# Kernel tuning notes

Hardware: AMD Instinct MI355X
Metric: run time of the kernel (lower is better)

The kernel has to match this reference:

```python
import jax, jax.numpy as jnp
import numpy as np

D_IN, HID, HEADS, MAXN, OUT, B = 16, 128, 4, 8, 128, 32768
HD = HID // HEADS
EPS = 1e-5


def _ln(x, g, b):
    m = jnp.mean(x, -1, keepdims=True)
    v = jnp.mean((x - m) ** 2, -1, keepdims=True)
    return (x - m) * jax.lax.rsqrt(v + EPS) * g + b


def _encode(x, enc_w1, enc_b1, enc_g1, enc_be1, enc_w2, enc_b2, enc_g2, enc_be2):
    h = _ln(x @ enc_w1.T + enc_b1, enc_g1, enc_be1)
    h = jax.nn.relu(h)
    return _ln(h @ enc_w2.T + enc_b2, enc_g2, enc_be2)


def setup_inputs() -> dict:
    key = jax.random.key(0)
    ks = jax.random.split(key, 12)

    def xavier(k, shape):
        # xavier_uniform with gain=0.5, matching _init_weights
        lim = 0.5 * np.sqrt(6.0 / (shape[0] + shape[1]))
        return jax.random.uniform(k, shape, jnp.float32, -lim, lim)

    z = lambda n: jnp.zeros((n,), jnp.float32)
    o = lambda n: jnp.ones((n,), jnp.float32)
    return {
        "current_node": jax.random.normal(ks[0], (B, D_IN), jnp.float32),
        "neighbor_nodes": jax.random.normal(ks[1], (B, MAXN, D_IN), jnp.float32),
        "neighbor_mask": jax.random.randint(ks[2], (B, MAXN), 0, 2, jnp.int32),
        "enc_w1": xavier(ks[3], (HID, D_IN)), "enc_b1": z(HID),
        "enc_g1": o(HID), "enc_be1": z(HID),
        "enc_w2": xavier(ks[4], (HID, HID)), "enc_b2": z(HID),
        "enc_g2": o(HID), "enc_be2": z(HID),
        "in_proj_w": xavier(ks[5], (3 * HID, HID)), "in_proj_b": z(3 * HID),
        "out_w": xavier(ks[6], (HID, HID)), "out_b": z(HID),
        "an_g": o(HID), "an_b": z(HID),
        "p1_w": xavier(ks[7], (HID, 2 * HID)), "p1_b": z(HID),
        "p1_g": o(HID), "p1_be": z(HID),
        "p2_w": xavier(ks[8], (OUT, HID)), "p2_b": z(OUT),
        "p2_g": o(OUT), "p2_be": z(OUT),
    }


def _forward(current_node, neighbor_nodes, neighbor_mask,
             enc_w1, enc_b1, enc_g1, enc_be1, enc_w2, enc_b2, enc_g2, enc_be2,
             in_proj_w, in_proj_b, out_w, out_b, an_g, an_b,
             p1_w, p1_b, p1_g, p1_be, p2_w, p2_b, p2_g, p2_be):
    bsz = current_node.shape[0]
    cur_emb = _encode(current_node, enc_w1, enc_b1, enc_g1, enc_be1,
                      enc_w2, enc_b2, enc_g2, enc_be2)                  # [B, HID]
    nb_emb = _encode(neighbor_nodes, enc_w1, enc_b1, enc_g1, enc_be1,
                     enc_w2, enc_b2, enc_g2, enc_be2)                   # [B, N, HID]

    valid = neighbor_mask > 0                                            # [B, N]
    has_nb = jnp.any(valid, axis=1)                                      # [B]

    # MultiheadAttention (eval mode, dropout inactive): q from current node, k/v from neighbors
    wq, wk, wv = in_proj_w[:HID], in_proj_w[HID:2 * HID], in_proj_w[2 * HID:]
    bq, bk, bv = in_proj_b[:HID], in_proj_b[HID:2 * HID], in_proj_b[2 * HID:]
    q = (cur_emb @ wq.T + bq).reshape(bsz, HEADS, HD)                    # [B, H, hd]
    k = (nb_emb @ wk.T + bk).reshape(bsz, MAXN, HEADS, HD)               # [B, N, H, hd]
    v = (nb_emb @ wv.T + bv).reshape(bsz, MAXN, HEADS, HD)

    scores = jnp.einsum('bhd,bnhd->bhn', q, k) / np.sqrt(HD)             # [B, H, N]
    # rows with zero valid neighbors get a fully-open mask to avoid NaN softmax;
    # their attention result is discarded below (replaced by cur_emb)
    safe = jnp.where(has_nb[:, None], valid, True)                       # [B, N]
    scores = jnp.where(safe[:, None, :], scores, -1e9)
    attn = jax.nn.softmax(scores, axis=-1)                               # [B, H, N]
    ctx = jnp.einsum('bhn,bnhd->bhd', attn, v).reshape(bsz, HID)
    ctx = ctx @ out_w.T + out_b
    agg = jnp.where(has_nb[:, None], _ln(ctx, an_g, an_b), cur_emb)      # [B, HID]

    combined = jnp.concatenate([cur_emb, agg], axis=-1)                  # [B, 2*HID]
    h = _ln(combined @ p1_w.T + p1_b, p1_g, p1_be)
    h = jax.nn.relu(h)
    return _ln(h @ p2_w.T + p2_b, p2_g, p2_be)                           # [B, OUT]


def reference(current_node, neighbor_nodes, neighbor_mask,
              enc_w1, enc_b1, enc_g1, enc_be1, enc_w2, enc_b2, enc_g2, enc_be2,
              in_proj_w, in_proj_b, out_w, out_b, an_g, an_b,
              p1_w, p1_b, p1_g, p1_be, p2_w, p2_b, p2_g, p2_be):
    return _forward(current_node, neighbor_nodes, neighbor_mask,
                    enc_w1, enc_b1, enc_g1, enc_be1, enc_w2, enc_b2, enc_g2, enc_be2,
                    in_proj_w, in_proj_b, out_w, out_b, an_g, an_b,
                    p1_w, p1_b, p1_g, p1_be, p2_w, p2_b, p2_g, p2_be)
```

## Files before the change

kernel.cpp:

```cpp
#include <hip/hip_runtime.h>

#define DEV __device__ __forceinline__

typedef __attribute__((ext_vector_type(8))) short bf16x8;
typedef __attribute__((ext_vector_type(4))) float f32x4;

static constexpr int NTH = 512;
static constexpr int TBE = 16;

static constexpr int W1P = 0;
static constexpr int W2  = 4096;
static constexpr int WQ  = 20480;
static constexpr int WK  = 36864;
static constexpr int WVW = 53248;
static constexpr int OW  = 69632;
static constexpr int P1A = 86016;
static constexpr int P1B = 102400;
static constexpr int P2W = 118784;
static constexpr int WS_BF16_TOT = 135168;
static constexpr int NPRM = 18 * 128;
static constexpr int WQr  = 139776;
static constexpr int OWr  = 156160;
static constexpr int P1Ar = 172544;
static constexpr int P1Br = 188928;
static constexpr int P2r  = 205312;
static constexpr int WKt  = 221696;
static constexpr int CURE = 238080;
static constexpr int NBE  = 238080 + 4194304;
static constexpr size_t SPLIT_NEED = (size_t)(NBE + 33554432) * 2;

DEV unsigned short f2bf(float f) {
  unsigned u = __float_as_uint(f);
  return (unsigned short)((u + 0x7fffu + ((u >> 16) & 1u)) >> 16);
}
DEV float bf2f(unsigned short u) { return __uint_as_float(((unsigned)u) << 16); }

DEV void st_bf16(unsigned short* buf, int row, int col, float v) {
  buf[row * 128 + ((((col >> 3) ^ (row & 7)) << 3) | (col & 7))] = f2bf(v);
}
DEV float ld_bf16(const unsigned short* buf, int row, int col) {
  unsigned u = buf[row * 128 + ((((col >> 3) ^ (row & 7)) << 3) | (col & 7))];
  return __uint_as_float(u << 16);
}
DEV bf16x8 frag128(const unsigned short* buf, int row, int kk, int lg) {
  return *(const bf16x8*)(buf + row * 128 + (((kk * 4 + lg) ^ (row & 7)) << 3));
}
DEV bf16x8 frag32(const unsigned short* buf, int row, int lg) {
  return *(const bf16x8*)(buf + row * 32 + ((lg ^ (row & 3)) << 3));
}
DEV f32x4 mfma16(bf16x8 a, bf16x8 b, f32x4 c) {
  return __builtin_amdgcn_mfma_f32_16x16x32_bf16(a, b, c, 0, 0, 0);
}

__global__ void prep(const float* __restrict__ enc_w1, const float* __restrict__ enc_w2,
                     const float* __restrict__ in_pw, const float* __restrict__ out_w,
                     const float* __restrict__ p1_w, const float* __restrict__ p2_w,
                     const float* __restrict__ enc_b1, const float* __restrict__ enc_g1,
                     const float* __restrict__ enc_be1, const float* __restrict__ enc_b2,
                     const float* __restrict__ enc_g2, const float* __restrict__ enc_be2,
                     const float* __restrict__ in_pb, const float* __restrict__ out_b,
                     const float* __restrict__ an_g, const float* __restrict__ an_b,
                     const float* __restrict__ p1_b, const float* __restrict__ p1_g,
                     const float* __restrict__ p1_be, const float* __restrict__ p2_b,
                     const float* __restrict__ p2_g, const float* __restrict__ p2_be,
                     unsigned short* __restrict__ wsb, float* __restrict__ wsp, int rm) {
  int t = blockIdx.x * blockDim.x + threadIdx.x;
  int NT = gridDim.x * blockDim.x;
  for (int i = t; i < 8 * 16384; i += NT) {
    int mi = i >> 14, e = i & 16383, row = e >> 7, col = e & 127;
    float v; int dstb;
    switch (mi) {
      case 0: v = enc_w2[row * 128 + col];         dstb = W2;  break;
      case 1: v = in_pw[row * 128 + col];          dstb = WQ;  break;
      case 2: v = in_pw[(128 + row) * 128 + col];  dstb = WK;  break;
      case 3: v = in_pw[(256 + row) * 128 + col];  dstb = WVW; break;
      case 4: v = out_w[row * 128 + col];          dstb = OW;  break;
      case 5: v = p1_w[row * 256 + col];           dstb = P1A; break;
      case 6: v = p1_w[row * 256 + 128 + col];     dstb = P1B; break;
      default: v = p2_w[row * 128 + col];          dstb = P2W; break;
    }
    wsb[dstb + row * 128 + ((((col >> 3) ^ (row & 7)) << 3) | (col & 7))] = f2bf(v);
  }
  for (int i = t; i < 4096; i += NT) {
    int row = i >> 5, col = i & 31;
    float v = (col < 16) ? enc_w1[row * 16 + col] : 0.f;
    wsb[W1P + row * 32 + ((((col >> 3) ^ (row & 3)) << 3) | (col & 7))] = f2bf(v);
  }
  if (rm) {
    for (int i = t; i < 6 * 16384; i += NT) {
      int mi = i >> 14, e = i & 16383, row = e >> 7, col = e & 127;
      float v; int dstb;
      switch (mi) {
        case 0: v = in_pw[row * 128 + col];         dstb = WQr;  break;
        case 1: v = out_w[row * 128 + col];         dstb = OWr;  break;
        case 2: v = p1_w[row * 256 + col];          dstb = P1Ar; break;
        case 3: v = p1_w[row * 256 + 128 + col];    dstb = P1Br; break;
        case 4: v = p2_w[row * 128 + col];          dstb = P2r;  break;
        default: v = in_pw[(128 + col) * 128 + row]; dstb = WKt; break;
      }
      wsb[dstb + e] = f2bf(v);
    }
  }
  for (int i = t; i < NPRM; i += NT) {
    int s = i >> 7, c = i & 127; float v;
    switch (s) {
      case 0: v = enc_b1[c]; break;  case 1: v = enc_g1[c]; break;
      case 2: v = enc_be1[c]; break; case 3: v = enc_b2[c]; break;
      case 4: v = enc_g2[c]; break;  case 5: v = enc_be2[c]; break;
      case 6: v = in_pb[c]; break;   case 7: v = in_pb[128 + c]; break;
      case 8: v = in_pb[256 + c]; break; case 9: v = out_b[c]; break;
      case 10: v = an_g[c]; break;   case 11: v = an_b[c]; break;
      case 12: v = p1_b[c]; break;   case 13: v = p1_g[c]; break;
      case 14: v = p1_be[c]; break;  case 15: v = p2_b[c]; break;
      case 16: v = p2_g[c]; break;   default: v = p2_be[c]; break;
    }
    wsp[i] = v;
  }
}

__global__ __launch_bounds__(512, 4)
void k1_enc(const float* __restrict__ cur_x, const float* __restrict__ nb_x,
            const unsigned short* __restrict__ wsb, const float* __restrict__ wsp,
            unsigned short* __restrict__ wse) {
  __shared__ __align__(16) unsigned short s_w1[4096];
  __shared__ __align__(16) unsigned short s_w2[16384];
  __shared__ __align__(16) unsigned short s_h1[8][16 * 136];
  __shared__ float s_prm[6 * 128];

  const int tid = threadIdx.x;
  const int wv = tid >> 6, l = tid & 63, l15 = l & 15, lg = l >> 4;

  ((uint4*)s_w1)[tid] = ((const uint4*)(wsb + W1P))[tid];
#pragma unroll
  for (int i = 0; i < 4; ++i)
    ((uint4*)s_w2)[tid + i * 512] = ((const uint4*)(wsb + W2))[tid + i * 512];
  for (int i = tid; i < 768; i += 512) s_prm[i] = wsp[i];
  __syncthreads();

  unsigned short* h1 = &s_h1[wv][0];

  auto ln_t = [&](float (&acc)[8][4], int bs, int gs, int es, bool relu) {
#pragma unroll
    for (int ct = 0; ct < 8; ++ct) {
      float4 bb = *(const float4*)&s_prm[bs * 128 + ct * 16 + lg * 4];
      acc[ct][0] += bb.x; acc[ct][1] += bb.y; acc[ct][2] += bb.z; acc[ct][3] += bb.w;
    }
    float sm = 0.f, sq = 0.f;
#pragma unroll
    for (int ct = 0; ct < 8; ++ct)
#pragma unroll
      for (int r = 0; r < 4; ++r) { sm += acc[ct][r]; sq = fmaf(acc[ct][r], acc[ct][r], sq); }
    sm += __shfl_xor(sm, 16); sq += __shfl_xor(sq, 16);
    sm += __shfl_xor(sm, 32); sq += __shfl_xor(sq, 32);
    float mean = sm * 0.0078125f;
    float var = fmaf(sq, 0.0078125f, -mean * mean);
    float inv = rsqrtf(var + 1e-5f);
#pragma unroll
    for (int ct = 0; ct < 8; ++ct) {
      float4 gg = *(const float4*)&s_prm[gs * 128 + ct * 16 + lg * 4];
      float4 ee = *(const float4*)&s_prm[es * 128 + ct * 16 + lg * 4];
      float ga[4] = {gg.x, gg.y, gg.z, gg.w}, ea[4] = {ee.x, ee.y, ee.z, ee.w};
#pragma unroll
      for (int r = 0; r < 4; ++r) {
        float v = (acc[ct][r] - mean) * inv * ga[r] + ea[r];
        acc[ct][r] = relu ? fmaxf(v, 0.f) : v;
      }
    }
  };

#pragma unroll 1
  for (int t = blockIdx.x * 8 + wv; t < 18432; t += 9216) {
    asm volatile("s_waitcnt lgkmcnt(0)" ::: "memory");
    const bool isnb = t < 16384;
    const float* src = isnb ? nb_x + (size_t)t * 256
                            : cur_x + ((size_t)t - 16384) * 256;
    unsigned short* dst = wse + (isnb ? (size_t)NBE + (size_t)t * 2048
                                      : (size_t)CURE + ((size_t)t - 16384) * 2048);

    float4 fin = ((const float4*)src)[l];
    {
      uint2 u;
      u.x = (unsigned)f2bf(fin.x) | ((unsigned)f2bf(fin.y) << 16);
      u.y = (unsigned)f2bf(fin.z) | ((unsigned)f2bf(fin.w) << 16);
      *(uint2*)(h1 + (l >> 2) * 16 + (l & 3) * 4) = u;
    }
    bf16x8 bx = (bf16x8){0, 0, 0, 0, 0, 0, 0, 0};
    if (lg < 2) bx = *(const bf16x8*)(h1 + l15 * 16 + lg * 8);

    float acc[8][4];
#pragma unroll
    for (int ct = 0; ct < 8; ++ct) {
      f32x4 a = {0.f, 0.f, 0.f, 0.f};
      a = mfma16(frag32(s_w1, ct * 16 + l15, lg), bx, a);
      acc[ct][0] = a[0]; acc[ct][1] = a[1]; acc[ct][2] = a[2]; acc[ct][3] = a[3];
    }
    ln_t(acc, 0, 1, 2, true);
#pragma unroll
    for (int ct = 0; ct < 8; ++ct) {
      uint2 u;
      u.x = (unsigned)f2bf(acc[ct][0]) | ((unsigned)f2bf(acc[ct][1]) << 16);
      u.y = (unsigned)f2bf(acc[ct][2]) | ((unsigned)f2bf(acc[ct][3]) << 16);
      *(uint2*)(h1 + l15 * 136 + ct * 16 + lg * 4) = u;
    }

    bf16x8 bh[4];
#pragma unroll
    for (int kk = 0; kk < 4; ++kk)
      bh[kk] = *(const bf16x8*)(h1 + l15 * 136 + kk * 32 + lg * 8);
#pragma unroll
    for (int ct = 0; ct < 8; ++ct) {
      f32x4 a = {0.f, 0.f, 0.f, 0.f};
#pragma unroll
      for (int kk = 0; kk < 4; ++kk)
        a = mfma16(frag128(s_w2, ct * 16 + l15, kk, lg), bh[kk], a);
      acc[ct][0] = a[0]; acc[ct][1] = a[1]; acc[ct][2] = a[2]; acc[ct][3] = a[3];
    }
    ln_t(acc, 3, 4, 5, false);

#pragma unroll
    for (int ct = 0; ct < 8; ++ct) {
      uint2 u;
      u.x = (unsigned)f2bf(acc[ct][0]) | ((unsigned)f2bf(acc[ct][1]) << 16);
      u.y = (unsigned)f2bf(acc[ct][2]) | ((unsigned)f2bf(acc[ct][3]) << 16);
      int c = ct * 2 + (lg >> 1);
      *(uint2*)(h1 + l15 * 128 + ((c ^ l15) << 3) + (lg & 1) * 4) = u;
    }
#pragma unroll
    for (int i = 0; i < 4; ++i) {
      int R = i * 4 + lg;
      int j = l15;
      uint4 u = *(const uint4*)(h1 + R * 128 + ((j ^ R) << 3));
      ((uint4*)dst)[i * 64 + l] = u;
    }
  }
}

__global__ __launch_bounds__(256, 2)
void k2_head(const int* __restrict__ nb_mask,
             const unsigned short* __restrict__ wsb, const float* __restrict__ wsp,
             float* __restrict__ out) {
  __shared__ __align__(16) unsigned char smem[47936];
  unsigned short* s_stage = (unsigned short*)smem;
  float*          s_f     = (float*)smem;
  unsigned short* s_agg   = (unsigned short*)(smem + 8448);
  unsigned short* s_q     = (unsigned short*)(smem + 32768);
  unsigned short* s_hh    = (unsigned short*)(smem + 32768);
  unsigned short* s_cur   = (unsigned short*)(smem + 37120);
  unsigned short* s_ctx   = (unsigned short*)(smem + 41472);
  float*          s_p     = (float*)(smem + 45824);
  int*            s_mask  = (int*)(smem + 47872);

  const int tid = threadIdx.x;
  const int wv = tid >> 6, l = tid & 63, l15 = l & 15, lg = l >> 4;
  const int ebase = blockIdx.x * TBE;

  {
    int row = tid >> 4, chunk = tid & 15;
    ((uint4*)s_cur)[row * 17 + chunk] = ((const uint4*)(wsb + CURE))[(size_t)ebase * 16 + tid];
  }
  if (tid < 16) {
    int m = 0; const int* mp = nb_mask + (size_t)(ebase + tid) * 8;
#pragma unroll
    for (int n = 0; n < 8; ++n) m |= (mp[n] > 0) << n;
    s_mask[tid] = m;
  }
  __syncthreads();

  {
    bf16x8 a[4];
#pragma unroll
    for (int kk = 0; kk < 4; ++kk)
      a[kk] = *(const bf16x8*)(wsb + CURE + ((size_t)(ebase + l15)) * 128 + kk * 32 + lg * 8);
#pragma unroll
    for (int u = 0; u < 2; ++u) {
      int nt = wv * 2 + u;
      f32x4 acc = {0.f, 0.f, 0.f, 0.f};
#pragma unroll
      for (int kk = 0; kk < 4; ++kk) {
        bf16x8 b = *(const bf16x8*)(wsb + WQr + (nt * 16 + l15) * 128 + kk * 32 + lg * 8);
        acc = mfma16(a[kk], b, acc);
      }
      int c = nt * 16 + l15;
      float bq = wsp[6 * 128 + c];
#pragma unroll
      for (int r = 0; r < 4; ++r)
        s_q[(lg * 4 + r) * 136 + c] = f2bf((acc[r] + bq) * 0.17677669529663687f);
    }
  }
#pragma unroll
  for (int i = 0; i < 8; ++i)
    ((uint4*)s_stage)[tid + i * 256] = ((const uint4*)(wsb + WK))[tid + i * 256];
  __syncthreads();

#pragma unroll 1
  for (int mi = 0; mi < 2; ++mi) {
    int mt = wv * 2 + mi;
    int el = mt * 2 + (lg >> 1);
    bf16x8 a[4];
#pragma unroll
    for (int kk = 0; kk < 4; ++kk)
      a[kk] = *(const bf16x8*)(wsb + NBE + ((size_t)ebase * 8 + mt * 16 + l15) * 128 + kk * 32 + lg * 8);
    float sacc[4][4];
#pragma unroll
    for (int h = 0; h < 4; ++h)
#pragma unroll
      for (int r = 0; r < 4; ++r) sacc[h][r] = 0.f;
#pragma unroll
    for (int nt = 0; nt < 8; ++nt) {
      f32x4 k4 = {0.f, 0.f, 0.f, 0.f};
#pragma unroll
      for (int kk = 0; kk < 4; ++kk)
        k4 = mfma16(a[kk], frag128(s_stage, nt * 16 + l15, kk, lg), k4);
      float qv = bf2f(s_q[el * 136 + nt * 16 + l15]);
      int h = nt >> 1;
#pragma unroll
      for (int r = 0; r < 4; ++r) sacc[h][r] = fmaf(k4[r], qv, sacc[h][r]);
    }
#pragma unroll
    for (int off = 1; off <= 8; off <<= 1)
#pragma unroll
      for (int h = 0; h < 4; ++h)
#pragma unroll
        for (int r = 0; r < 4; ++r) sacc[h][r] += __shfl_xor(sacc[h][r], off);
    int m = s_mask[el];
    int nbase = (lg & 1) * 4;
    float p[4][4];
#pragma unroll
    for (int h = 0; h < 4; ++h) {
      float mx = -1e30f;
#pragma unroll
      for (int r = 0; r < 4; ++r) {
        bool use = (m == 0) || ((m >> (nbase + r)) & 1);
        mx = fmaxf(mx, use ? sacc[h][r] : -1e30f);
      }
      mx = fmaxf(mx, __shfl_xor(mx, 16));
      float sum = 0.f;
#pragma unroll
      for (int r = 0; r < 4; ++r) {
        bool use = (m == 0) || ((m >> (nbase + r)) & 1);
        p[h][r] = use ? __expf(sacc[h][r] - mx) : 0.f;
        sum += p[h][r];
      }
      sum += __shfl_xor(sum, 16);
      float inv = 1.f / sum;
#pragma unroll
      for (int r = 0; r < 4; ++r) p[h][r] *= inv;
    }
    if (l15 == 0) {
#pragma unroll
      for (int h = 0; h < 4; ++h)
#pragma unroll
        for (int r = 0; r < 4; ++r) s_p[el * 32 + h * 8 + nbase + r] = p[h][r];
    }
  }
  __syncthreads();
#pragma unroll
  for (int i = 0; i < 8; ++i)
    ((uint4*)s_stage)[tid + i * 256] = ((const uint4*)(wsb + WVW))[tid + i * 256];
  __syncthreads();

#pragma unroll 1
  for (int mi = 0; mi < 2; ++mi) {
    int mt = wv * 2 + mi;
    int el = mt * 2 + (lg >> 1);
    bf16x8 a[4];
#pragma unroll
    for (int kk = 0; kk < 4; ++kk)
      a[kk] = *(const bf16x8*)(wsb + NBE + ((size_t)ebase * 8 + mt * 16 + l15) * 128 + kk * 32 + lg * 8);
    float4 p4[4];
#pragma unroll
    for (int h = 0; h < 4; ++h)
      p4[h] = *(const float4*)&s_p[el * 32 + h * 8 + (lg & 1) * 4];
    float cacc[8];
#pragma unroll
    for (int nt = 0; nt < 8; ++nt) {
      f32x4 v4 = {0.f, 0.f, 0.f, 0.f};
#pragma unroll
      for (int kk = 0; kk < 4; ++kk)
        v4 = mfma16(a[kk], frag128(s_stage, nt * 16 + l15, kk, lg), v4);
      int h = nt >> 1;
      cacc[nt] = p4[h].x * v4[0] + p4[h].y * v4[1] + p4[h].z * v4[2] + p4[h].w * v4[3];
    }
#pragma unroll
    for (int nt = 0; nt < 8; ++nt) cacc[nt] += __shfl_xor(cacc[nt], 16);
    if ((lg & 1) == 0) {
#pragma unroll
      for (int nt = 0; nt < 8; ++nt) {
        int c = nt * 16 + l15;
        s_ctx[el * 136 + c] = f2bf(cacc[nt] + wsp[8 * 128 + c]);
      }
    }
  }
  __syncthreads();

  {
    bf16x8 a[4];
#pragma unroll
    for (int kk = 0; kk < 4; ++kk)
      a[kk] = *(const bf16x8*)(s_ctx + l15 * 136 + kk * 32 + lg * 8);
#pragma unroll
    for (int u = 0; u < 2; ++u) {
      int nt = wv * 2 + u;
      f32x4 acc = {0.f, 0.f, 0.f, 0.f};
#pragma unroll
      for (int kk = 0; kk < 4; ++kk) {
        bf16x8 b = *(const bf16x8*)(wsb + OWr + (nt * 16 + l15) * 128 + kk * 32 + lg * 8);
        acc = mfma16(a[kk], b, acc);
      }
      int c = nt * 16 + l15;
      float bo = wsp[9 * 128 + c];
#pragma unroll
      for (int r = 0; r < 4; ++r) s_f[(lg * 4 + r) * 132 + c] = acc[r] + bo;
    }
  }
  __syncthreads();

  {
    int eo = wv * 4 + (l >> 4);
    float4 x0 = *(const float4*)&s_f[eo * 132 + l15 * 8];
    float4 x1 = *(const float4*)&s_f[eo * 132 + l15 * 8 + 4];
    float xa[8] = {x0.x, x0.y, x0.z, x0.w, x1.x, x1.y, x1.z, x1.w};
    float sm = 0.f, sq = 0.f;
#pragma unroll
    for (int j = 0; j < 8; ++j) { sm += xa[j]; sq = fmaf(xa[j], xa[j], sq); }
#pragma unroll
    for (int off = 1; off <= 8; off <<= 1) { sm += __shfl_xor(sm, off); sq += __shfl_xor(sq, off); }
    float mean = sm * 0.0078125f;
    float var = fmaf(sq, 0.0078125f, -mean * mean);
    float inv = rsqrtf(var + 1e-5f);
    int m = s_mask[eo];
    unsigned short o8[8];
    const unsigned short* cu = s_cur + eo * 136 + l15 * 8;
#pragma unroll
    for (int j = 0; j < 8; ++j) {
      int c = l15 * 8 + j;
      float v = (xa[j] - mean) * inv * wsp[10 * 128 + c] + wsp[11 * 128 + c];
      o8[j] = m ? f2bf(v) : cu[j];
    }
    uint4 u;
    u.x = (unsigned)o8[0] | ((unsigned)o8[1] << 16);
    u.y = (unsigned)o8[2] | ((unsigned)o8[3] << 16);
    u.z = (unsigned)o8[4] | ((unsigned)o8[5] << 16);
    u.w = (unsigned)o8[6] | ((unsigned)o8[7] << 16);
    *(uint4*)(s_agg + eo * 136 + l15 * 8) = u;
  }
  __syncthreads();

  {
    bf16x8 ac[4], ag[4];
#pragma unroll
    for (int kk = 0; kk < 4; ++kk) {
      ac[kk] = *(const bf16x8*)(s_cur + l15 * 136 + kk * 32 + lg * 8);
      ag[kk] = *(const bf16x8*)(s_agg + l15 * 136 + kk * 32 + lg * 8);
    }
#pragma unroll
    for (int u = 0; u < 2; ++u) {
      int nt = wv * 2 + u;
      f32x4 acc = {0.f, 0.f, 0.f, 0.f};
#pragma unroll
      for (int kk = 0; kk < 4; ++kk) {
        bf16x8 b = *(const bf16x8*)(wsb + P1Ar + (nt * 16 + l15) * 128 + kk * 32 + lg * 8);
        acc = mfma16(ac[kk], b, acc);
      }
#pragma unroll
      for (int kk = 0; kk < 4; ++kk) {
        bf16x8 b = *(const bf16x8*)(wsb + P1Br + (nt * 16 + l15) * 128 + kk * 32 + lg * 8);
        acc = mfma16(ag[kk], b, acc);
      }
      int c = nt * 16 + l15;
      float bb = wsp[12 * 128 + c];
#pragma unroll
      for (int r = 0; r < 4; ++r) s_f[(lg * 4 + r) * 132 + c] = acc[r] + bb;
    }
  }
  __syncthreads();

  {
    int eo = wv * 4 + (l >> 4);
    float4 x0 = *(const float4*)&s_f[eo * 132 + l15 * 8];
    float4 x1 = *(const float4*)&s_f[eo * 132 + l15 * 8 + 4];
    float xa[8] = {x0.x, x0.y, x0.z, x0.w, x1.x, x1.y, x1.z, x1.w};
    float sm = 0.f, sq = 0.f;
#pragma unroll
    for (int j = 0; j < 8; ++j) { sm += xa[j]; sq = fmaf(xa[j], xa[j], sq); }
#pragma unroll
    for (int off = 1; off <= 8; off <<= 1) { sm += __shfl_xor(sm, off); sq += __shfl_xor(sq, off); }
    float mean = sm * 0.0078125f;
    float var = fmaf(sq, 0.0078125f, -mean * mean);
    float inv = rsqrtf(var + 1e-5f);
    unsigned short o8[8];
#pragma unroll
    for (int j = 0; j < 8; ++j) {
      int c = l15 * 8 + j;
      float v = (xa[j] - mean) * inv * wsp[13 * 128 + c] + wsp[14 * 128 + c];
      o8[j] = f2bf(fmaxf(v, 0.f));
    }
    uint4 u;
    u.x = (unsigned)o8[0] | ((unsigned)o8[1] << 16);
    u.y = (unsigned)o8[2] | ((unsigned)o8[3] << 16);
    u.z = (unsigned)o8[4] | ((unsigned)o8[5] << 16);
    u.w = (unsigned)o8[6] | ((unsigned)o8[7] << 16);
    *(uint4*)(s_hh + eo * 136 + l15 * 8) = u;
  }
  __syncthreads();

  {
    bf16x8 a[4];
#pragma unroll
    for (int kk = 0; kk < 4; ++kk)
      a[kk] = *(const bf16x8*)(s_hh + l15 * 136 + kk * 32 + lg * 8);
#pragma unroll
    for (int u = 0; u < 2; ++u) {
      int nt = wv * 2 + u;
      f32x4 acc = {0.f, 0.f, 0.f, 0.f};
#pragma unroll
      for (int kk = 0; kk < 4; ++kk) {
        bf16x8 b = *(const bf16x8*)(wsb + P2r + (nt * 16 + l15) * 128 + kk * 32 + lg * 8);
        acc = mfma16(a[kk], b, acc);
      }
      int c = nt * 16 + l15;
      float bb = wsp[15 * 128 + c];
#pragma unroll
      for (int r = 0; r < 4; ++r) s_f[(lg * 4 + r) * 132 + c] = acc[r] + bb;
    }
  }
  __syncthreads();

  {
    int eo = wv * 4 + (l >> 4);
    float4 x0 = *(const float4*)&s_f[eo * 132 + l15 * 8];
    float4 x1 = *(const float4*)&s_f[eo * 132 + l15 * 8 + 4];
    float xa[8] = {x0.x, x0.y, x0.z, x0.w, x1.x, x1.y, x1.z, x1.w};
    float sm = 0.f, sq = 0.f;
#pragma unroll
    for (int j = 0; j < 8; ++j) { sm += xa[j]; sq = fmaf(xa[j], xa[j], sq); }
#pragma unroll
    for (int off = 1; off <= 8; off <<= 1) { sm += __shfl_xor(sm, off); sq += __shfl_xor(sq, off); }
    float mean = sm * 0.0078125f;
    float var = fmaf(sq, 0.0078125f, -mean * mean);
    float inv = rsqrtf(var + 1e-5f);
    float o[8];
#pragma unroll
    for (int j = 0; j < 8; ++j) {
      int c = l15 * 8 + j;
      o[j] = (xa[j] - mean) * inv * wsp[16 * 128 + c] + wsp[17 * 128 + c];
    }
    float* op = out + (size_t)(ebase + eo) * 128 + l15 * 8;
    *(float4*)op = make_float4(o[0], o[1], o[2], o[3]);
    *(float4*)(op + 4) = make_float4(o[4], o[5], o[6], o[7]);
  }
}

__global__ __launch_bounds__(NTH, 1)
void gcn_mfma(const float* __restrict__ cur_x, const float* __restrict__ nb_x,
              const int* __restrict__ nb_mask,
              const unsigned short* __restrict__ wsb, const float* __restrict__ wsp,
              float* __restrict__ out) {
  __shared__ __align__(16) unsigned short s_stage[20480];
  __shared__ __align__(16) unsigned short s_X[144 * 32];
  __shared__ __align__(16) unsigned short s_H[144 * 128];
  __shared__ __align__(16) unsigned short s_Enb[128 * 128];
  __shared__ __align__(16) unsigned short s_Ecur[16 * 128];
  __shared__ __align__(16) float s_q[16 * 132];
  __shared__ __align__(16) float s_p[16 * 32];
  __shared__ __align__(16) unsigned short s_ctx[16 * 128];
  __shared__ __align__(16) unsigned short s_agg[16 * 128];
  __shared__ __align__(16) unsigned short s_hh[16 * 128];
  __shared__ float s_prm[NPRM];
  __shared__ int s_mask[16];

  const int tid = threadIdx.x;
  const int wv = tid >> 6, l = tid & 63, l15 = l & 15, lg = l >> 4;
  const int sub = l >> 5, l32 = l & 31;
  const int ebase = blockIdx.x * TBE;
  const int eo = wv * 2 + sub;

  auto stage = [&](int srcOff) {
    const uint4* s = (const uint4*)(wsb + srcOff);
    uint4* d = (uint4*)s_stage;
#pragma unroll
    for (int i = 0; i < 4; ++i) d[tid + i * NTH] = s[tid + i * NTH];
  };
  auto ln_epi = [&](float (&vals)[8][4], int bslot, int gslot, int beslot, bool relu) {
    float sm[4] = {0, 0, 0, 0}, sq[4] = {0, 0, 0, 0};
#pragma unroll
    for (int nt = 0; nt < 8; ++nt) {
      float b = s_prm[bslot * 128 + nt * 16 + l15];
#pragma unroll
      for (int r = 0; r < 4; ++r) {
        float v = vals[nt][r] + b; vals[nt][r] = v;
        sm[r] += v; sq[r] = fmaf(v, v, sq[r]);
      }
    }
#pragma unroll
    for (int off = 8; off >= 1; off >>= 1)
#pragma unroll
      for (int r = 0; r < 4; ++r) {
        sm[r] += __shfl_xor(sm[r], off);
        sq[r] += __shfl_xor(sq[r], off);
      }
    float mean[4], inv[4];
#pragma unroll
    for (int r = 0; r < 4; ++r) {
      mean[r] = sm[r] * 0.0078125f;
      float var = fmaf(sq[r], 0.0078125f, -mean[r] * mean[r]);
      inv[r] = rsqrtf(var + 1e-5f);
    }
#pragma unroll
    for (int nt = 0; nt < 8; ++nt) {
      int col = nt * 16 + l15;
      float g = s_prm[gslot * 128 + col], be = s_prm[beslot * 128 + col];
#pragma unroll
      for (int r = 0; r < 4; ++r) {
        float v = (vals[nt][r] - mean[r]) * inv[r] * g + be;
        vals[nt][r] = relu ? fmaxf(v, 0.f) : v;
      }
    }
  };

  {
    const uint4* s = (const uint4*)(wsb + W1P);
    ((uint4*)(s_stage + 16384))[tid] = s[tid];
  }
  for (int i = tid; i < NPRM; i += NTH) s_prm[i] = wsp[i];
  for (int i = tid; i < 4608; i += NTH) {
    int row = i >> 5, col = i & 31;
    int e = (row * 57) >> 9, kind = row - e * 9;
    float v = 0.f;
    if (col < 16) {
      int ge = ebase + e;
      v = (kind == 0) ? cur_x[(size_t)ge * 16 + col]
                      : nb_x[((size_t)ge * 8 + (kind - 1)) * 16 + col];
    }
    s_X[row * 32 + ((((col >> 3) ^ (row & 3)) << 3) | (col & 7))] = f2bf(v);
  }
  if (tid < 16) {
    int m = 0; const int* mp = nb_mask + (size_t)(ebase + tid) * 8;
#pragma unroll
    for (int n = 0; n < 8; ++n) m |= (mp[n] > 0) << n;
    s_mask[tid] = m;
  }
  __syncthreads();

  stage(W2);
  for (int mt = wv; mt < 9; mt += 8) {
    bf16x8 a = frag32(s_X, mt * 16 + l15, lg);
    float vals[8][4];
#pragma unroll
    for (int nt = 0; nt < 8; ++nt) {
      f32x4 acc = {0.f, 0.f, 0.f, 0.f};
      acc = mfma16(a, frag32(s_stage + 16384, nt * 16 + l15, lg), acc);
#pragma unroll
      for (int r = 0; r < 4; ++r) vals[nt][r] = acc[r];
    }
    ln_epi(vals, 0, 1, 2, true);
#pragma unroll
    for (int nt = 0; nt < 8; ++nt)
#pragma unroll
      for (int r = 0; r < 4; ++r)
        st_bf16(s_H, mt * 16 + lg * 4 + r, nt * 16 + l15, vals[nt][r]);
  }
  __syncthreads();

  for (int mt = wv; mt < 9; mt += 8) {
    bf16x8 a[4];
#pragma unroll
    for (int kk = 0; kk < 4; ++kk) a[kk] = frag128(s_H, mt * 16 + l15, kk, lg);
    float vals[8][4];
#pragma unroll
    for (int nt = 0; nt < 8; ++nt) {
      f32x4 acc = {0.f, 0.f, 0.f, 0.f};
#pragma unroll
      for (int kk = 0; kk < 4; ++kk)
        acc = mfma16(a[kk], frag128(s_stage, nt * 16 + l15, kk, lg), acc);
#pragma unroll
      for (int r = 0; r < 4; ++r) vals[nt][r] = acc[r];
    }
    ln_epi(vals, 3, 4, 5, false);
#pragma unroll
    for (int nt = 0; nt < 8; ++nt) {
      int col = nt * 16 + l15;
#pragma unroll
      for (int r = 0; r < 4; ++r) {
        int R = mt * 16 + lg * 4 + r;
        int e = (R * 57) >> 9, kind = R - e * 9;
        if (kind == 0) st_bf16(s_Ecur, e, col, vals[nt][r]);
        else           st_bf16(s_Enb, e * 8 + kind - 1, col, vals[nt][r]);
      }
    }
  }
  __syncthreads();
  stage(WQ);
  __syncthreads();

  {
    f32x4 acc = {0.f, 0.f, 0.f, 0.f};
#pragma unroll
    for (int kk = 0; kk < 4; ++kk)
      acc = mfma16(frag128(s_Ecur, l15, kk, lg), frag128(s_stage, wv * 16 + l15, kk, lg), acc);
    int col = wv * 16 + l15; float bq = s_prm[6 * 128 + col];
#pragma unroll
    for (int r = 0; r < 4; ++r) s_q[(lg * 4 + r) * 132 + col] = acc[r] + bq;
  }
  __syncthreads();
  stage(WK);
  __syncthreads();

  {
    bf16x8 b[4];
#pragma unroll
    for (int kk = 0; kk < 4; ++kk) b[kk] = frag128(s_stage, wv * 16 + l15, kk, lg);
    int col = wv * 16 + l15; float bk = s_prm[7 * 128 + col];
#pragma unroll
    for (int mt = 0; mt < 8; ++mt) {
      f32x4 acc = {0.f, 0.f, 0.f, 0.f};
#pragma unroll
      for (int kk = 0; kk < 4; ++kk)
        acc = mfma16(frag128(s_Enb, mt * 16 + l15, kk, lg), b[kk], acc);
#pragma unroll
      for (int r = 0; r < 4; ++r)
        st_bf16(s_H, mt * 16 + lg * 4 + r, col, acc[r] + bk);
    }
  }
  __syncthreads();

  stage(WVW);
  {
    int h = l32 >> 3, n = l32 & 7;
    int krow = eo * 8 + n;
    float dot = 0.f;
#pragma unroll
    for (int j = 0; j < 4; ++j) {
      bf16x8 kf = *(const bf16x8*)(s_H + krow * 128 + (((h * 4 + j) ^ (krow & 7)) << 3));
      const float* qp = s_q + eo * 132 + h * 32 + j * 8;
      float4 q0 = *(const float4*)qp, q1 = *(const float4*)(qp + 4);
      dot = fmaf(__uint_as_float(((unsigned)(unsigned short)kf[0]) << 16), q0.x, dot);
      dot = fmaf(__uint_as_float(((unsigned)(unsigned short)kf[1]) << 16), q0.y, dot);
      dot = fmaf(__uint_as_float(((unsigned)(unsigned short)kf[2]) << 16), q0.z, dot);
      dot = fmaf(__uint_as_float(((unsigned)(unsigned short)kf[3]) << 16), q0.w, dot);
      dot = fmaf(__uint_as_float(((unsigned)(unsigned short)kf[4]) << 16), q1.x, dot);
      dot = fmaf(__uint_as_float(((unsigned)(unsigned short)kf[5]) << 16), q1.y, dot);
      dot = fmaf(__uint_as_float(((unsigned)(unsigned short)kf[6]) << 16), q1.z, dot);
      dot = fmaf(__uint_as_float(((unsigned)(unsigned short)kf[7]) << 16), q1.w, dot);
    }
    float sc = dot * 0.17677669529663687f;
    int m = s_mask[eo];
    bool use = (m == 0) || ((m >> n) & 1);
    float scm = use ? sc : -1e30f;
    float mx = scm;
#pragma unroll
    for (int off = 4; off >= 1; off >>= 1) mx = fmaxf(mx, __shfl_xor(mx, off));
    float p = use ? __expf(sc - mx) : 0.f;
    float sum = p;
#pragma unroll
    for (int off = 4; off >= 1; off >>= 1) sum += __shfl_xor(sum, off);
    s_p[eo * 32 + h * 8 + n] = p / sum;
  }
  __syncthreads();

  {
    bf16x8 b[4];
#pragma unroll
    for (int kk = 0; kk < 4; ++kk) b[kk] = frag128(s_stage, wv * 16 + l15, kk, lg);
    int col = wv * 16 + l15; float bv = s_prm[8 * 128 + col];
#pragma unroll
    for (int mt = 0; mt < 8; ++mt) {
      f32x4 acc = {0.f, 0.f, 0.f, 0.f};
#pragma unroll
      for (int kk = 0; kk < 4; ++kk)
        acc = mfma16(frag128(s_Enb, mt * 16 + l15, kk, lg), b[kk], acc);
#pragma unroll
      for (int r = 0; r < 4; ++r)
        st_bf16(s_H, mt * 16 + lg * 4 + r, col, acc[r] + bv);
    }
  }
  __syncthreads();

  stage(OW);
  {
#pragma unroll
    for (int cc = 0; cc < 4; ++cc) {
      int col = l32 + 32 * cc;
      float c = 0.f;
#pragma unroll
      for (int n = 0; n < 8; ++n)
        c = fmaf(s_p[eo * 32 + cc * 8 + n], ld_bf16(s_H, eo * 8 + n, col), c);
      st_bf16(s_ctx, eo, col, c);
    }
  }
  __syncthreads();

  {
    f32x4 acc = {0.f, 0.f, 0.f, 0.f};
#pragma unroll
    for (int kk = 0; kk < 4; ++kk)
      acc = mfma16(frag128(s_ctx, l15, kk, lg), frag128(s_stage, wv * 16 + l15, kk, lg), acc);
    int col = wv * 16 + l15; float bo = s_prm[9 * 128 + col];
#pragma unroll
    for (int r = 0; r < 4; ++r) s_q[(lg * 4 + r) * 132 + col] = acc[r] + bo;
  }
  __syncthreads();

  stage(P1A);
  {
    float4 x = *(const float4*)&s_q[eo * 132 + l32 * 4];
    float s = x.x + x.y + x.z + x.w;
    float qq = fmaf(x.x, x.x, fmaf(x.y, x.y, fmaf(x.z, x.z, x.w * x.w)));
#pragma unroll
    for (int off = 16; off >= 1; off >>= 1) { s += __shfl_xor(s, off); qq += __shfl_xor(qq, off); }
    float mean = s * 0.0078125f;
    float var = fmaf(qq, 0.0078125f, -mean * mean);
    float inv = rsqrtf(var + 1e-5f);
    int m = s_mask[eo];
    float xa[4] = {x.x, x.y, x.z, x.w}, r4[4];
#pragma unroll
    for (int c = 0; c < 4; ++c) {
      int col = l32 * 4 + c;
      float v = (xa[c] - mean) * inv * s_prm[10 * 128 + col] + s_prm[11 * 128 + col];
      r4[c] = m ? v : ld_bf16(s_Ecur, eo, col);
    }
    uint2 uu;
    uu.x = (unsigned)f2bf(r4[0]) | ((unsigned)f2bf(r4[1]) << 16);
    uu.y = (unsigned)f2bf(r4[2]) | ((unsigned)f2bf(r4[3]) << 16);
    *(uint2*)(s_agg + eo * 128 + (((l32 >> 1) ^ (eo & 7)) << 3) + (l32 & 1) * 4) = uu;
  }
  __syncthreads();

  f32x4 accP = {0.f, 0.f, 0.f, 0.f};
#pragma unroll
  for (int kk = 0; kk < 4; ++kk)
    accP = mfma16(frag128(s_Ecur, l15, kk, lg), frag128(s_stage, wv * 16 + l15, kk, lg), accP);
  __syncthreads();
  stage(P1B);
  __syncthreads();
  {
#pragma unroll
    for (int kk = 0; kk < 4; ++kk)
      accP = mfma16(frag128(s_agg, l15, kk, lg), frag128(s_stage, wv * 16 + l15, kk, lg), accP);
    int col = wv * 16 + l15; float b = s_prm[12 * 128 + col];
#pragma unroll
    for (int r = 0; r < 4; ++r) s_q[(lg * 4 + r) * 132 + col] = accP[r] + b;
  }
  __syncthreads();

  stage(P2W);
  {
    float4 x = *(const float4*)&s_q[eo * 132 + l32 * 4];
    float s = x.x + x.y + x.z + x.w;
    float qq = fmaf(x.x, x.x, fmaf(x.y, x.y, fmaf(x.z, x.z, x.w * x.w)));
#pragma unroll
    for (int off = 16; off >= 1; off >>= 1) { s += __shfl_xor(s, off); qq += __shfl_xor(qq, off); }
    float mean = s * 0.0078125f;
    float var = fmaf(qq, 0.0078125f, -mean * mean);
    float inv = rsqrtf(var + 1e-5f);
    float xa[4] = {x.x, x.y, x.z, x.w}, r4[4];
#pragma unroll
    for (int c = 0; c < 4; ++c) {
      int col = l32 * 4 + c;
      r4[c] = fmaxf((xa[c] - mean) * inv * s_prm[13 * 128 + col] + s_prm[14 * 128 + col], 0.f);
    }
    uint2 uu;
    uu.x = (unsigned)f2bf(r4[0]) | ((unsigned)f2bf(r4[1]) << 16);
    uu.y = (unsigned)f2bf(r4[2]) | ((unsigned)f2bf(r4[3]) << 16);
    *(uint2*)(s_hh + eo * 128 + (((l32 >> 1) ^ (eo & 7)) << 3) + (l32 & 1) * 4) = uu;
  }
  __syncthreads();

  {
    f32x4 acc = {0.f, 0.f, 0.f, 0.f};
#pragma unroll
    for (int kk = 0; kk < 4; ++kk)
      acc = mfma16(frag128(s_hh, l15, kk, lg), frag128(s_stage, wv * 16 + l15, kk, lg), acc);
    int col = wv * 16 + l15; float b = s_prm[15 * 128 + col];
#pragma unroll
    for (int r = 0; r < 4; ++r) s_q[(lg * 4 + r) * 132 + col] = acc[r] + b;
  }
  __syncthreads();

  {
    float4 x = *(const float4*)&s_q[eo * 132 + l32 * 4];
    float s = x.x + x.y + x.z + x.w;
    float qq = fmaf(x.x, x.x, fmaf(x.y, x.y, fmaf(x.z, x.z, x.w * x.w)));
#pragma unroll
    for (int off = 16; off >= 1; off >>= 1) { s += __shfl_xor(s, off); qq += __shfl_xor(qq, off); }
    float mean = s * 0.0078125f;
    float var = fmaf(qq, 0.0078125f, -mean * mean);
    float inv = rsqrtf(var + 1e-5f);
    float xa[4] = {x.x, x.y, x.z, x.w};
    float4 o;
    o.x = (xa[0] - mean) * inv * s_prm[16 * 128 + l32 * 4 + 0] + s_prm[17 * 128 + l32 * 4 + 0];
    o.y = (xa[1] - mean) * inv * s_prm[16 * 128 + l32 * 4 + 1] + s_prm[17 * 128 + l32 * 4 + 1];
    o.z = (xa[2] - mean) * inv * s_prm[16 * 128 + l32 * 4 + 2] + s_prm[17 * 128 + l32 * 4 + 2];
    o.w = (xa[3] - mean) * inv * s_prm[16 * 128 + l32 * 4 + 3] + s_prm[17 * 128 + l32 * 4 + 3];
    *(float4*)&out[(size_t)(ebase + eo) * 128 + l32 * 4] = o;
  }
}

extern "C" void kernel_launch(void* const* d_in, const int* in_sizes, int n_in,
                              void* d_out, int out_size, void* d_ws, size_t ws_size,
                              hipStream_t stream) {
  const float* cur_x   = (const float*)d_in[0];
  const float* nb_x    = (const float*)d_in[1];
  const int*   nbm     = (const int*)d_in[2];
  const float* enc_w1  = (const float*)d_in[3];
  const float* enc_b1  = (const float*)d_in[4];
  const float* enc_g1  = (const float*)d_in[5];
  const float* enc_be1 = (const float*)d_in[6];
  const float* enc_w2  = (const float*)d_in[7];
  const float* enc_b2  = (const float*)d_in[8];
  const float* enc_g2  = (const float*)d_in[9];
  const float* enc_be2 = (const float*)d_in[10];
  const float* in_pw   = (const float*)d_in[11];
  const float* in_pb   = (const float*)d_in[12];
  const float* out_w   = (const float*)d_in[13];
  const float* out_b   = (const float*)d_in[14];
  const float* an_g    = (const float*)d_in[15];
  const float* an_b    = (const float*)d_in[16];
  const float* p1_w    = (const float*)d_in[17];
  const float* p1_b    = (const float*)d_in[18];
  const float* p1_g    = (const float*)d_in[19];
  const float* p1_be   = (const float*)d_in[20];
  const float* p2_w    = (const float*)d_in[21];
  const float* p2_b    = (const float*)d_in[22];
  const float* p2_g    = (const float*)d_in[23];
  const float* p2_be   = (const float*)d_in[24];
  float* out = (float*)d_out;

  unsigned short* wsb = (unsigned short*)d_ws;
  float* wsp = (float*)(wsb + WS_BF16_TOT);
  const int B = in_sizes[0] / 16;
  const bool split = (ws_size >= SPLIT_NEED) && (B == 32768);

  prep<<<128, 256, 0, stream>>>(enc_w1, enc_w2, in_pw, out_w, p1_w, p2_w,
                                enc_b1, enc_g1, enc_be1, enc_b2, enc_g2, enc_be2,
                                in_pb, out_b, an_g, an_b, p1_b, p1_g, p1_be,
                                p2_b, p2_g, p2_be, wsb, wsp, split ? 1 : 0);

  if (split) {
    k1_enc<<<1152, 512, 0, stream>>>(cur_x, nb_x, wsb, wsp, wsb);
    k2_head<<<B / TBE, 256, 0, stream>>>(nbm, wsb, wsp, out);
  } else {
    gcn_mfma<<<B / TBE, NTH, 0, stream>>>(cur_x, nb_x, nbm, wsb, wsp, out);
  }
}
```

Baseline: 134.7 us.

## Reassociate attention: fold Wk into query and Wv after weighted neighbor sum

Instead of projecting every neighbor embedding through Wk and Wv with MFMA, the head kernel now maps q through Wk^T per head and dots that with raw neighbor embeddings. It forms the probability-weighted neighbor sum per head, then applies Wv once per element. This divides the K/V projection work by the neighbor count. Neighbor embeddings are staged once into shared memory, which replaces the weight staging and raises the LDS footprint, possibly hurting occupancy. It adds scalar FMA work and an extra bf16 rounding of intermediates. The bias on K cancels in softmax and the V bias passes through, so the results should match.

Result: no change. 137.1 us (+1.8%).

```diff
diff --git a/kernel.cpp b/kernel.cpp
--- a/kernel.cpp
+++ b/kernel.cpp
@@ -239,16 +239,17 @@
 void k2_head(const int* __restrict__ nb_mask,
              const unsigned short* __restrict__ wsb, const float* __restrict__ wsp,
              float* __restrict__ out) {
-  __shared__ __align__(16) unsigned char smem[47936];
-  unsigned short* s_stage = (unsigned short*)smem;
-  float*          s_f     = (float*)smem;
-  unsigned short* s_agg   = (unsigned short*)(smem + 8448);
-  unsigned short* s_q     = (unsigned short*)(smem + 32768);
-  unsigned short* s_hh    = (unsigned short*)(smem + 32768);
-  unsigned short* s_cur   = (unsigned short*)(smem + 37120);
-  unsigned short* s_ctx   = (unsigned short*)(smem + 41472);
-  float*          s_p     = (float*)(smem + 45824);
-  int*            s_mask  = (int*)(smem + 47872);
+  __shared__ __align__(16) unsigned char smem[62272];
+  unsigned short* s_nb  = (unsigned short*)smem;
+  float*          s_f   = (float*)smem;
+  unsigned short* s_agg = (unsigned short*)(smem + 8448);
+  unsigned short* s_qk  = (unsigned short*)(smem + 32768);
+  unsigned short* s_pnb = (unsigned short*)(smem + 32768);
+  unsigned short* s_q   = (unsigned short*)(smem + 49152);
+  unsigned short* s_hh  = (unsigned short*)(smem + 49152);
+  unsigned short* s_cur = (unsigned short*)(smem + 53504);
+  unsigned short* s_ctx = (unsigned short*)(smem + 57856);
+  int*            s_mask = (int*)(smem + 62208);
 
   const int tid = threadIdx.x;
   const int wv = tid >> 6, l = tid & 63, l15 = l & 15, lg = l >> 4;
@@ -258,6 +259,12 @@
     int row = tid >> 4, chunk = tid & 15;
     ((uint4*)s_cur)[row * 17 + chunk] = ((const uint4*)(wsb + CURE))[(size_t)ebase * 16 + tid];
   }
+  {
+    const uint4* src = (const uint4*)(wsb + NBE + (size_t)ebase * 1024);
+#pragma unroll
+    for (int i = 0; i < 8; ++i)
+      ((uint4*)s_nb)[i * 256 + tid] = src[i * 256 + tid];
+  }
   if (tid < 16) {
     int m = 0; const int* mp = nb_mask + (size_t)(ebase + tid) * 8;
 #pragma unroll
@@ -287,108 +294,130 @@
         s_q[(lg * 4 + r) * 136 + c] = f2bf((acc[r] + bq) * 0.17677669529663687f);
     }
   }
-#pragma unroll
-  for (int i = 0; i < 8; ++i)
-    ((uint4*)s_stage)[tid + i * 256] = ((const uint4*)(wsb + WK))[tid + i * 256];
-  __syncthreads();
-
-#pragma unroll 1
-  for (int mi = 0; mi < 2; ++mi) {
-    int mt = wv * 2 + mi;
-    int el = mt * 2 + (lg >> 1);
-    bf16x8 a[4];
-#pragma unroll
-    for (int kk = 0; kk < 4; ++kk)
-      a[kk] = *(const bf16x8*)(wsb + NBE + ((size_t)ebase * 8 + mt * 16 + l15) * 128 + kk * 32 + lg * 8);
-    float sacc[4][4];
+  __builtin_amdgcn_sched_barrier(0);
+
+  {
+    bf16x8 qb = *(const bf16x8*)(s_q + l15 * 136 + wv * 32 + lg * 8);
+    __builtin_amdgcn_sched_barrier(0);
+#pragma unroll
+    for (int ct = 0; ct < 8; ++ct) {
+      bf16x8 w = *(const bf16x8*)(wsb + WKt + (ct * 16 + l15) * 128 + wv * 32 + lg * 8);
+      f32x4 a4 = {0.f, 0.f, 0.f, 0.f};
+      a4 = mfma16(w, qb, a4);
+      uint2 uu;
+      uu.x = (unsigned)f2bf(a4[0]) | ((unsigned)f2bf(a4[1]) << 16);
+      uu.y = (unsigned)f2bf(a4[2]) | ((unsigned)f2bf(a4[3]) << 16);
+      *(uint2*)(s_qk + l15 * 512 + wv * 128 + ct * 16 + lg * 4) = uu;
+    }
+  }
+  __syncthreads();
+
+  float p[4][8];
+  {
+    const int e = wv * 4 + lg;
+    const int c0 = l15 * 8;
+    float qf[4][8];
+#pragma unroll
+    for (int h = 0; h < 4; ++h) {
+      bf16x8 q8 = *(const bf16x8*)(s_qk + e * 512 + h * 128 + c0);
+#pragma unroll
+      for (int i = 0; i < 8; ++i) qf[h][i] = bf2f((unsigned short)q8[i]);
+    }
+    float sp[4][8];
 #pragma unroll
     for (int h = 0; h < 4; ++h)
 #pragma unroll
-      for (int r = 0; r < 4; ++r) sacc[h][r] = 0.f;
-#pragma unroll
-    for (int nt = 0; nt < 8; ++nt) {
-      f32x4 k4 = {0.f, 0.f, 0.f, 0.f};
-#pragma unroll
-      for (int kk = 0; kk < 4; ++kk)
-        k4 = mfma16(a[kk], frag128(s_stage, nt * 16 + l15, kk, lg), k4);
-      float qv = bf2f(s_q[el * 136 + nt * 16 + l15]);
-      int h = nt >> 1;
-#pragma unroll
-      for (int r = 0; r < 4; ++r) sacc[h][r] = fmaf(k4[r], qv, sacc[h][r]);
-    }
-#pragma unroll
-    for (int off = 1; off <= 8; off <<= 1)
-#pragma unroll
-      for (int h = 0; h < 4; ++h)
-#pragma unroll
-        for (int r = 0; r < 4; ++r) sacc[h][r] += __shfl_xor(sacc[h][r], off);
-    int m = s_mask[el];
-    int nbase = (lg & 1) * 4;
-    float p[4][4];
+      for (int n = 0; n < 8; ++n) sp[h][n] = 0.f;
+#pragma unroll
+    for (int n = 0; n < 8; ++n) {
+      bf16x8 nb8 = *(const bf16x8*)(s_nb + (e * 8 + n) * 128 + c0);
+#pragma unroll
+      for (int i = 0; i < 8; ++i) {
+        float v = bf2f((unsigned short)nb8[i]);
+#pragma unroll
+        for (int h = 0; h < 4; ++h) sp[h][n] = fmaf(qf[h][i], v, sp[h][n]);
+      }
+    }
+#pragma unroll
+    for (int h = 0; h < 4; ++h)
+#pragma unroll
+      for (int n = 0; n < 8; ++n) {
+        sp[h][n] += __shfl_xor(sp[h][n], 1);
+        sp[h][n] += __shfl_xor(sp[h][n], 2);
+        sp[h][n] += __shfl_xor(sp[h][n], 4);
+        sp[h][n] += __shfl_xor(sp[h][n], 8);
+      }
+    int m = s_mask[e];
+    bool all = (m == 0);
 #pragma unroll
     for (int h = 0; h < 4; ++h) {
       float mx = -1e30f;
 #pragma unroll
-      for (int r = 0; r < 4; ++r) {
-        bool use = (m == 0) || ((m >> (nbase + r)) & 1);
-        mx = fmaxf(mx, use ? sacc[h][r] : -1e30f);
-      }
-      mx = fmaxf(mx, __shfl_xor(mx, 16));
-      float sum = 0.f;
-#pragma unroll
-      for (int r = 0; r < 4; ++r) {
-        bool use = (m == 0) || ((m >> (nbase + r)) & 1);
-        p[h][r] = use ? __expf(sacc[h][r] - mx) : 0.f;
-        sum += p[h][r];
-      }
-      sum += __shfl_xor(sum, 16);
-      float inv = 1.f / sum;
-#pragma unroll
-      for (int r = 0; r < 4; ++r) p[h][r] *= inv;
-    }
-    if (l15 == 0) {
-#pragma unroll
-      for (int h = 0; h < 4; ++h)
-#pragma unroll
-        for (int r = 0; r < 4; ++r) s_p[el * 32 + h * 8 + nbase + r] = p[h][r];
-    }
-  }
-  __syncthreads();
-#pragma unroll
-  for (int i = 0; i < 8; ++i)
-    ((uint4*)s_stage)[tid + i * 256] = ((const uint4*)(wsb + WVW))[tid + i * 256];
-  __syncthreads();
-
-#pragma unroll 1
-  for (int mi = 0; mi < 2; ++mi) {
-    int mt = wv * 2 + mi;
-    int el = mt * 2 + (lg >> 1);
-    bf16x8 a[4];
+      for (int n = 0; n < 8; ++n) {
+        bool u = all || ((m >> n) & 1);
+        mx = fmaxf(mx, u ? sp[h][n] : -1e30f);
+      }
+      float su = 0.f;
+#pragma unroll
+      for (int n = 0; n < 8; ++n) {
+        bool u = all || ((m >> n) & 1);
+        p[h][n] = u ? __expf(sp[h][n] - mx) : 0.f;
+        su += p[h][n];
+      }
+      float inv = 1.f / su;
+#pragma unroll
+      for (int n = 0; n < 8; ++n) p[h][n] *= inv;
+    }
+  }
+  __syncthreads();
+
+  {
+    const int e = wv * 4 + lg;
+    const int c0 = l15 * 8;
+    float pn[4][8];
+#pragma unroll
+    for (int h = 0; h < 4; ++h)
+#pragma unroll
+      for (int i = 0; i < 8; ++i) pn[h][i] = 0.f;
+#pragma unroll
+    for (int n = 0; n < 8; ++n) {
+      bf16x8 nb8 = *(const bf16x8*)(s_nb + (e * 8 + n) * 128 + c0);
+#pragma unroll
+      for (int i = 0; i < 8; ++i) {
+        float v = bf2f((unsigned short)nb8[i]);
+#pragma unroll
+        for (int h = 0; h < 4; ++h) pn[h][i] = fmaf(p[h][n], v, pn[h][i]);
+      }
+    }
+#pragma unroll
+    for (int h = 0; h < 4; ++h) {
+      uint4 u;
+      u.x = (unsigned)f2bf(pn[h][0]) | ((unsigned)f2bf(pn[h][1]) << 16);
+      u.y = (unsigned)f2bf(pn[h][2]) | ((unsigned)f2bf(pn[h][3]) << 16);
+      u.z = (unsigned)f2bf(pn[h][4]) | ((unsigned)f2bf(pn[h][5]) << 16);
+      u.w = (unsigned)f2bf(pn[h][6]) | ((unsigned)f2bf(pn[h][7]) << 16);
+      *(uint4*)(s_pnb + e * 512 + h * 128 + c0) = u;
+    }
+  }
+  __syncthreads();
+
+  {
+    bf16x8 b[4];
 #pragma unroll
     for (int kk = 0; kk < 4; ++kk)
-      a[kk] = *(const bf16x8*)(wsb + NBE + ((size_t)ebase * 8 + mt * 16 + l15) * 128 + kk * 32 + lg * 8);
-    float4 p4[4];
-#pragma unroll
-    for (int h = 0; h < 4; ++h)
-      p4[h] = *(const float4*)&s_p[el * 32 + h * 8 + (lg & 1) * 4];
-    float cacc[8];
-#pragma unroll
-    for (int nt = 0; nt < 8; ++nt) {
-      f32x4 v4 = {0.f, 0.f, 0.f, 0.f};
+      b[kk] = *(const bf16x8*)(s_pnb + l15 * 512 + wv * 128 + kk * 32 + lg * 8);
+#pragma unroll
+    for (int u = 0; u < 2; ++u) {
+      int ct = wv * 2 + u;
+      f32x4 a4 = {0.f, 0.f, 0.f, 0.f};
 #pragma unroll
       for (int kk = 0; kk < 4; ++kk)
-        v4 = mfma16(a[kk], frag128(s_stage, nt * 16 + l15, kk, lg), v4);
-      int h = nt >> 1;
-      cacc[nt] = p4[h].x * v4[0] + p4[h].y * v4[1] + p4[h].z * v4[2] + p4[h].w * v4[3];
-    }
-#pragma unroll
-    for (int nt = 0; nt < 8; ++nt) cacc[nt] += __shfl_xor(cacc[nt], 16);
-    if ((lg & 1) == 0) {
-#pragma unroll
-      for (int nt = 0; nt < 8; ++nt) {
-        int c = nt * 16 + l15;
-        s_ctx[el * 136 + c] = f2bf(cacc[nt] + wsp[8 * 128 + c]);
-      }
+        a4 = mfma16(frag128(wsb + WVW, ct * 16 + l15, kk, lg), b[kk], a4);
+      float4 bb = *(const float4*)&wsp[8 * 128 + ct * 16 + lg * 4];
+      uint2 uu;
+      uu.x = (unsigned)f2bf(a4[0] + bb.x) | ((unsigned)f2bf(a4[1] + bb.y) << 16);
+      uu.y = (unsigned)f2bf(a4[2] + bb.z) | ((unsigned)f2bf(a4[3] + bb.w) << 16);
+      *(uint2*)(s_ctx + l15 * 136 + ct * 16 + lg * 4) = uu;
     }
   }
   __syncthreads();
```
